# Performance work log

Hardware: AMD Instinct MI355X
Metric: run time of the kernel (lower is better)

Reference implementation:

```python
import jax, jax.numpy as jnp
import numpy as np

N_NODES = 50000
N_EDGES = 800000
D_IN, D_H, D_E = 512, 512, 256


def setup_inputs() -> dict:
    key = jax.random.key(0)
    ks = jax.random.split(key, 16)

    def lin(kw, kb, fan_in, fan_out):
        s = 1.0 / np.sqrt(fan_in)
        W = jax.random.uniform(kw, (fan_in, fan_out), dtype=jnp.float32, minval=-s, maxval=s)
        b = jax.random.uniform(kb, (fan_out,), dtype=jnp.float32, minval=-s, maxval=s)
        return W, b

    W1, b1 = lin(ks[2], ks[3], D_IN, D_H)
    W2, b2 = lin(ks[4], ks[5], D_H, D_H)
    W3, b3 = lin(ks[6], ks[7], D_H, D_E)
    We, be = lin(ks[8], ks[9], D_E, 7)
    Wh, bh = lin(ks[10], ks[11], D_E, 8)
    Wg, bg = lin(ks[12], ks[13], D_E, 57)

    return {
        "x": jax.random.normal(ks[0], (N_NODES, D_IN), dtype=jnp.float32),
        "edge_index": jax.random.randint(ks[1], (2, N_EDGES), 0, N_NODES, dtype=jnp.int32),
        "W1": W1, "b1": b1, "W2": W2, "b2": b2, "W3": W3, "b3": b3,
        "We": We, "be": be, "Wh": Wh, "bh": bh, "Wg": Wg, "bg": bg,
    }


def reference(x, edge_index, W1, b1, W2, b2, W3, b3, We, be, Wh, bh, Wg, bg):
    n = x.shape[0]
    # GCNConv: add self-loops, symmetric normalization D^{-1/2} A D^{-1/2}
    loops = jnp.arange(n, dtype=edge_index.dtype)
    src = jnp.concatenate([edge_index[0], loops])  # message sources
    dst = jnp.concatenate([edge_index[1], loops])  # aggregation targets
    deg = jax.ops.segment_sum(jnp.ones_like(src, dtype=x.dtype), dst, num_segments=n)
    dis = jnp.where(deg > 0, jax.lax.rsqrt(deg), 0.0)
    norm = (dis[src] * dis[dst])[:, None]  # [E+N, 1]

    def gcn_conv(h, W, b):
        h = h @ W                                   # [n, d_out]
        msg = h[src] * norm                         # gather + scale
        return jax.ops.segment_sum(msg, dst, num_segments=n) + b

    h = jax.nn.relu(gcn_conv(x, W1, b1))
    h = jax.nn.relu(gcn_conv(h, W2, b2))
    emb = gcn_conv(h, W3, b3)
    employment = emb @ We + be
    healthcare = emb @ Wh + bh
    grocery = emb @ Wg + bg
    return emb, employment, healthcare, grocery
```

## Files before the change

kernel.cpp:

```cpp
#include <hip/hip_runtime.h>

#define NN   50000
#define NNP  50048
#define NE   800000
#define DIN  512
#define DH   512
#define DE   256

#define CSR_CAP 1150016

typedef __bf16 bf16_t;
typedef __bf16 bf16x4 __attribute__((ext_vector_type(4)));
typedef __bf16 bf16x8 __attribute__((ext_vector_type(8)));
typedef float  f32x4  __attribute__((ext_vector_type(4)));
typedef _Float16 half_t;
typedef _Float16 half8 __attribute__((ext_vector_type(8)));

#define PB_SPLIT 25024
#define PB_IDEG  3125
#define PB_CSR   1124
#define PB_W1    1024
#define PB_W2    1024
#define PB_W3    512
#define PB_HEADW 80
#define PB_TOTAL (PB_SPLIT + PB_IDEG + PB_CSR + PB_W1 + PB_W2 + PB_W3 + PB_HEADW)

__global__ void k_prep(const float* __restrict__ X, bf16_t* __restrict__ Xh,
                       bf16_t* __restrict__ Xl, const int* __restrict__ dst,
                       int* __restrict__ indeg, int* __restrict__ csr,
                       const float* __restrict__ W1, bf16_t* __restrict__ B1h, bf16_t* __restrict__ B1l,
                       const float* __restrict__ W2, half_t* __restrict__ B2h, half_t* __restrict__ B2l,
                       const float* __restrict__ W3, half_t* __restrict__ B3h, half_t* __restrict__ B3l,
                       const float* __restrict__ We, const float* __restrict__ be,
                       const float* __restrict__ Wh, const float* __restrict__ bh,
                       const float* __restrict__ Wg, const float* __restrict__ bg,
                       bf16_t* __restrict__ Wth, bf16_t* __restrict__ Wtl,
                       float* __restrict__ bc) {
    int b = blockIdx.x;
    if (b < PB_SPLIT) {
        long idx = (long)b * 256 + threadIdx.x;
        long base = idx * 4;
        int row = (int)(base >> 9);
        f32x4 v;
        if (row < NN) v = *(const f32x4*)(X + base);
        else { v[0] = 0.f; v[1] = 0.f; v[2] = 0.f; v[3] = 0.f; }
        bf16x4 h, l;
        #pragma unroll
        for (int c = 0; c < 4; ++c) {
            float f = v[c];
            bf16_t hh = (bf16_t)f;
            h[c] = hh;
            l[c] = (bf16_t)(f - (float)hh);
        }
        *(bf16x4*)(Xh + base) = h;
        *(bf16x4*)(Xl + base) = l;
        return;
    }
    b -= PB_SPLIT;
    if (b < PB_IDEG) {
        int i = b * 256 + threadIdx.x;
        atomicAdd(&indeg[dst[i]], 1);
        return;
    }
    b -= PB_IDEG;
    if (b < PB_CSR) {
        int i = b * 256 + threadIdx.x;
        if (i < CSR_CAP / 4) ((int4*)csr)[i] = make_int4(NN, NN, NN, NN);
        return;
    }
    b -= PB_CSR;
    if (b < PB_W1) {
        int idx = b * 256 + threadIdx.x;
        int k = idx >> 9, n = idx & 511;
        float f = W1[idx];
        bf16_t h = (bf16_t)f;
        B1h[(size_t)n * DIN + k] = h;
        B1l[(size_t)n * DIN + k] = (bf16_t)(f - (float)h);
        return;
    }
    b -= PB_W1;
    if (b < PB_W2) {
        int idx = b * 256 + threadIdx.x;
        int k = idx >> 9, n = idx & 511;
        float f = W2[idx];
        half_t h = (half_t)f;
        B2h[(size_t)n * DH + k] = h;
        B2l[(size_t)n * DH + k] = (half_t)((f - (float)h) * 4096.f);
        return;
    }
    b -= PB_W2;
    if (b < PB_W3) {
        int idx = b * 256 + threadIdx.x;
        int k = idx >> 8, n = idx & 255;
        float f = W3[idx];
        half_t h = (half_t)f;
        B3h[(size_t)n * DH + k] = h;
        B3l[(size_t)n * DH + k] = (half_t)((f - (float)h) * 4096.f);
        return;
    }
    b -= PB_W3;
    {
        int idx = b * 256 + threadIdx.x;
        int n = idx / 256, k = idx % 256;
        float f = 0.f;
        if (n < 7)       f = We[k * 7 + n];
        else if (n < 15) f = Wh[k * 8 + (n - 7)];
        else if (n < 72) f = Wg[k * 57 + (n - 15)];
        bf16_t h = (bf16_t)f;
        Wth[idx] = h;
        Wtl[idx] = (bf16_t)(f - (float)h);
        if (k == 0) {
            float bb = 0.f;
            if (n < 7)       bb = be[n];
            else if (n < 15) bb = bh[n - 7];
            else if (n < 72) bb = bg[n - 15];
            bc[n] = bb;
        }
    }
}

#define SCAN_BLOCKS 49

__global__ __launch_bounds__(1024) void k_scan_a(const int* __restrict__ indeg,
                                                 int* __restrict__ rowptr,
                                                 float* __restrict__ dis,
                                                 int* __restrict__ bsum) {
    __shared__ int wsum[16];
    const int tid = threadIdx.x, lane = tid & 63, wid = tid >> 6;
    const int i = blockIdx.x * 1024 + tid;
    int deg = (i < NN) ? indeg[i] : 0;
    int v = (deg + 7) & ~7;
    int x = v;
    #pragma unroll
    for (int d = 1; d < 64; d <<= 1) {
        int t = __shfl_up(x, d, 64);
        if (lane >= d) x += t;
    }
    if (lane == 63) wsum[wid] = x;
    __syncthreads();
    if (wid == 0) {
        int s = (lane < 16) ? wsum[lane] : 0;
        #pragma unroll
        for (int d = 1; d < 16; d <<= 1) {
            int t = __shfl_up(s, d, 64);
            if (lane >= d) s += t;
        }
        if (lane < 16) wsum[lane] = s;
    }
    __syncthreads();
    int woff = (wid > 0) ? wsum[wid - 1] : 0;
    if (i < NN) {
        rowptr[i] = x - v + woff;
        dis[i] = rsqrtf((float)(deg + 1));
    } else if (i < NNP) {
        dis[i] = 0.f;
    }
    if (tid == 0) bsum[blockIdx.x] = wsum[15];
}

__global__ __launch_bounds__(64) void k_scan_b(const int* __restrict__ bsum,
                                               int* __restrict__ boff,
                                               int* __restrict__ rowptr) {
    const int lane = threadIdx.x;
    int v = (lane < SCAN_BLOCKS) ? bsum[lane] : 0;
    int x = v;
    #pragma unroll
    for (int d = 1; d < 64; d <<= 1) {
        int t = __shfl_up(x, d, 64);
        if (lane >= d) x += t;
    }
    if (lane < SCAN_BLOCKS) boff[lane] = x - v;
    if (lane == SCAN_BLOCKS - 1) rowptr[NN] = x;
}

__global__ void k_scan_c(const int* __restrict__ boff, int* __restrict__ rowptr,
                         int* __restrict__ cursor) {
    int i = blockIdx.x * blockDim.x + threadIdx.x;
    if (i < NN) {
        int r = rowptr[i] + boff[i >> 10];
        rowptr[i] = r;
        cursor[i] = r;
    }
}

__global__ void k_fill(const int* __restrict__ src, const int* __restrict__ dst,
                       int* __restrict__ cursor, int* __restrict__ csr, int e) {
    int i = blockIdx.x * blockDim.x + threadIdx.x;
    if (i < e) {
        int d = dst[i];
        int p = atomicAdd(&cursor[d], 1);
        csr[p] = src[i];
    }
}


__device__ __forceinline__ void gld_lds16(const void* g, void* l) {
    __builtin_amdgcn_global_load_lds(
        (const __attribute__((address_space(1))) unsigned int*)g,
        (__attribute__((address_space(3))) unsigned int*)l, 16, 0, 0);
}



__global__ __launch_bounds__(512) void k_gemm_bf3(
    const bf16_t* __restrict__ Ah, const bf16_t* __restrict__ Al,
    const bf16_t* __restrict__ Bh, const bf16_t* __restrict__ Bl,
    const float* __restrict__ disv,
    half_t* __restrict__ C, int N, int K) {
    __shared__ alignas(16) bf16_t sAh[2][128 * 32];
    __shared__ alignas(16) bf16_t sAl[2][128 * 32];
    __shared__ alignas(16) bf16_t sBh[2][128 * 32];
    __shared__ alignas(16) bf16_t sBl[2][128 * 32];

    const int tid = threadIdx.x;
    const int wave = tid >> 6, lane = tid & 63;
    const int quad = lane >> 4, l16 = lane & 15;
    const int bm = blockIdx.y * 128, bn = blockIdx.x * 128;
    const int wm = (wave >> 1) * 32, wn = (wave & 1) * 64;

    f32x4 acc[2][4];
    #pragma unroll
    for (int i = 0; i < 2; ++i)
        #pragma unroll
        for (int j = 0; j < 4; ++j)
            #pragma unroll
            for (int r = 0; r < 4; ++r) acc[i][j][r] = 0.f;

    const int srow = tid >> 2;
    const int schk = ((tid & 3) ^ ((tid >> 3) & 3)) * 16;
    const unsigned ldso = (unsigned)wave * 1024;

    const char* gAh0 = (const char*)(Ah + (size_t)(bm + srow) * K) + schk;
    const char* gAl0 = (const char*)(Al + (size_t)(bm + srow) * K) + schk;
    const char* gBh0 = (const char*)(Bh + (size_t)(bn + srow) * K) + schk;
    const char* gBl0 = (const char*)(Bl + (size_t)(bn + srow) * K) + schk;

    const int rsw = (l16 >> 1) & 3;
    const int nsteps = K >> 5;

    gld_lds16(gAh0, (char*)sAh[0] + ldso);
    gld_lds16(gAl0, (char*)sAl[0] + ldso);
    gld_lds16(gBh0, (char*)sBh[0] + ldso);
    gld_lds16(gBl0, (char*)sBl[0] + ldso);
    __syncthreads();

    for (int t = 0; t < nsteps; ++t) {
        const int cur = t & 1;
        if (t + 1 < nsteps) {
            const size_t kb = (size_t)(t + 1) * 64;
            const int nx = cur ^ 1;
            gld_lds16(gAh0 + kb, (char*)sAh[nx] + ldso);
            gld_lds16(gAl0 + kb, (char*)sAl[nx] + ldso);
            gld_lds16(gBh0 + kb, (char*)sBh[nx] + ldso);
            gld_lds16(gBl0 + kb, (char*)sBl[nx] + ldso);
        }
        bf16x8 fah[2], fal[2], fbh[4], fbl[4];
        #pragma unroll
        for (int i = 0; i < 2; ++i) {
            fah[i] = *(const bf16x8*)(sAh[cur] + (wm + 16 * i + l16) * 32 + (quad ^ rsw) * 8);
            fal[i] = *(const bf16x8*)(sAl[cur] + (wm + 16 * i + l16) * 32 + (quad ^ rsw) * 8);
        }
        #pragma unroll
        for (int j = 0; j < 4; ++j) {
            fbh[j] = *(const bf16x8*)(sBh[cur] + (wn + 16 * j + l16) * 32 + (quad ^ rsw) * 8);
            fbl[j] = *(const bf16x8*)(sBl[cur] + (wn + 16 * j + l16) * 32 + (quad ^ rsw) * 8);
        }
        #pragma unroll
        for (int i = 0; i < 2; ++i)
            #pragma unroll
            for (int j = 0; j < 4; ++j) {
                acc[i][j] = __builtin_amdgcn_mfma_f32_16x16x32_bf16(fah[i], fbh[j], acc[i][j], 0, 0, 0);
                acc[i][j] = __builtin_amdgcn_mfma_f32_16x16x32_bf16(fah[i], fbl[j], acc[i][j], 0, 0, 0);
                acc[i][j] = __builtin_amdgcn_mfma_f32_16x16x32_bf16(fal[i], fbh[j], acc[i][j], 0, 0, 0);
            }
        __syncthreads();
    }

    #pragma unroll
    for (int i = 0; i < 2; ++i) {
        const int rowb = bm + wm + 16 * i + quad * 4;
        float d0 = disv[rowb], d1 = disv[rowb + 1], d2 = disv[rowb + 2], d3 = disv[rowb + 3];
        #pragma unroll
        for (int j = 0; j < 4; ++j) {
            int col = bn + wn + 16 * j + l16;
            C[(size_t)(rowb + 0) * N + col] = (half_t)(acc[i][j][0] * d0);
            C[(size_t)(rowb + 1) * N + col] = (half_t)(acc[i][j][1] * d1);
            C[(size_t)(rowb + 2) * N + col] = (half_t)(acc[i][j][2] * d2);
            C[(size_t)(rowb + 3) * N + col] = (half_t)(acc[i][j][3] * d3);
        }
    }
}


__global__ __launch_bounds__(512) void k_gemm_f16(
    const half_t* __restrict__ A,
    const half_t* __restrict__ Bh, const half_t* __restrict__ Bl,
    const float* __restrict__ disv,
    half_t* __restrict__ C, int N, int K) {
    __shared__ alignas(16) half_t sA [2][128 * 32];
    __shared__ alignas(16) half_t sBh[2][128 * 32];
    __shared__ alignas(16) half_t sBl[2][128 * 32];

    const int tid = threadIdx.x;
    const int wave = tid >> 6, lane = tid & 63;
    const int quad = lane >> 4, l16 = lane & 15;
    const int bm = blockIdx.y * 128, bn = blockIdx.x * 128;
    const int wm = (wave >> 1) * 32, wn = (wave & 1) * 64;

    f32x4 aH[2][4], aM[2][4];
    #pragma unroll
    for (int i = 0; i < 2; ++i)
        #pragma unroll
        for (int j = 0; j < 4; ++j)
            #pragma unroll
            for (int r = 0; r < 4; ++r) { aH[i][j][r] = 0.f; aM[i][j][r] = 0.f; }

    const int srow = tid >> 2;
    const int schk = ((tid & 3) ^ ((tid >> 3) & 3)) * 16;
    const unsigned ldso = (unsigned)wave * 1024;

    const char* gA0  = (const char*)(A  + (size_t)(bm + srow) * K) + schk;
    const char* gBh0 = (const char*)(Bh + (size_t)(bn + srow) * K) + schk;
    const char* gBl0 = (const char*)(Bl + (size_t)(bn + srow) * K) + schk;

    const int rsw = (l16 >> 1) & 3;
    const int nsteps = K >> 5;

    gld_lds16(gA0,  (char*)sA[0]  + ldso);
    gld_lds16(gBh0, (char*)sBh[0] + ldso);
    gld_lds16(gBl0, (char*)sBl[0] + ldso);
    __syncthreads();

    for (int t = 0; t < nsteps; ++t) {
        const int cur = t & 1;
        if (t + 1 < nsteps) {
            const size_t kb = (size_t)(t + 1) * 64;
            const int nx = cur ^ 1;
            gld_lds16(gA0  + kb, (char*)sA[nx]  + ldso);
            gld_lds16(gBh0 + kb, (char*)sBh[nx] + ldso);
            gld_lds16(gBl0 + kb, (char*)sBl[nx] + ldso);
        }
        half8 fa[2], fbh[4], fbl[4];
        #pragma unroll
        for (int i = 0; i < 2; ++i)
            fa[i] = *(const half8*)(sA[cur] + (wm + 16 * i + l16) * 32 + (quad ^ rsw) * 8);
        #pragma unroll
        for (int j = 0; j < 4; ++j) {
            fbh[j] = *(const half8*)(sBh[cur] + (wn + 16 * j + l16) * 32 + (quad ^ rsw) * 8);
            fbl[j] = *(const half8*)(sBl[cur] + (wn + 16 * j + l16) * 32 + (quad ^ rsw) * 8);
        }
        #pragma unroll
        for (int i = 0; i < 2; ++i)
            #pragma unroll
            for (int j = 0; j < 4; ++j) {
                aH[i][j] = __builtin_amdgcn_mfma_f32_16x16x32_f16(fa[i], fbh[j], aH[i][j], 0, 0, 0);
                aM[i][j] = __builtin_amdgcn_mfma_f32_16x16x32_f16(fa[i], fbl[j], aM[i][j], 0, 0, 0);
            }
        __syncthreads();
    }

    const float s = 1.f / 4096.f;
    #pragma unroll
    for (int i = 0; i < 2; ++i) {
        const int rowb = bm + wm + 16 * i + quad * 4;
        float d0 = disv[rowb], d1 = disv[rowb + 1], d2 = disv[rowb + 2], d3 = disv[rowb + 3];
        #pragma unroll
        for (int j = 0; j < 4; ++j) {
            int col = bn + wn + 16 * j + l16;
            C[(size_t)(rowb + 0) * N + col] = (half_t)(fmaf(aM[i][j][0], s, aH[i][j][0]) * d0);
            C[(size_t)(rowb + 1) * N + col] = (half_t)(fmaf(aM[i][j][1], s, aH[i][j][1]) * d1);
            C[(size_t)(rowb + 2) * N + col] = (half_t)(fmaf(aM[i][j][2], s, aH[i][j][2]) * d2);
            C[(size_t)(rowb + 3) * N + col] = (half_t)(fmaf(aM[i][j][3], s, aH[i][j][3]) * d3);
        }
    }
}


__global__ __launch_bounds__(128) void k_agg16(
    const half_t* __restrict__ t, const int* __restrict__ rowptr,
    const int* __restrict__ csr, const float* __restrict__ dis,
    const float* __restrict__ bias, half_t* __restrict__ out) {
    const int node = blockIdx.x * 2 + (threadIdx.x >> 6);
    const int lane = threadIdx.x & 63;
    const int beg = rowptr[node], end = rowptr[node + 1];
    const float din = dis[node];
    const char* tc = (const char*)t;
    const unsigned lb = (unsigned)lane * 16u;

    float a0[8], a1[8], a2[8], a3[8];
    #pragma unroll
    for (int c = 0; c < 8; ++c) { a0[c] = 0.f; a1[c] = 0.f; a2[c] = 0.f; a3[c] = 0.f; }

    if (beg < end) {
        int4 sa = *(const int4*)(csr + beg);
        int4 sb = *(const int4*)(csr + beg + 4);
        half8 v0 = *(const half8*)(tc + (((unsigned)sa.x) << 10) + lb);
        half8 v1 = *(const half8*)(tc + (((unsigned)sa.y) << 10) + lb);
        half8 v2 = *(const half8*)(tc + (((unsigned)sa.z) << 10) + lb);
        half8 v3 = *(const half8*)(tc + (((unsigned)sa.w) << 10) + lb);
        half8 v4 = *(const half8*)(tc + (((unsigned)sb.x) << 10) + lb);
        half8 v5 = *(const half8*)(tc + (((unsigned)sb.y) << 10) + lb);
        half8 v6 = *(const half8*)(tc + (((unsigned)sb.z) << 10) + lb);
        half8 v7 = *(const half8*)(tc + (((unsigned)sb.w) << 10) + lb);
        int4 na = sa, nb = sb;
        if (beg + 8 < end) {
            na = *(const int4*)(csr + beg + 8);
            nb = *(const int4*)(csr + beg + 12);
        }
        for (int e = beg; e < end; ) {
            half8 u0 = v0, u1 = v1, u2 = v2, u3 = v3, u4 = v4, u5 = v5, u6 = v6, u7 = v7;
            e += 8;
            if (e < end) {
                v0 = *(const half8*)(tc + (((unsigned)na.x) << 10) + lb);
                v1 = *(const half8*)(tc + (((unsigned)na.y) << 10) + lb);
                v2 = *(const half8*)(tc + (((unsigned)na.z) << 10) + lb);
                v3 = *(const half8*)(tc + (((unsigned)na.w) << 10) + lb);
                v4 = *(const half8*)(tc + (((unsigned)nb.x) << 10) + lb);
                v5 = *(const half8*)(tc + (((unsigned)nb.y) << 10) + lb);
                v6 = *(const half8*)(tc + (((unsigned)nb.z) << 10) + lb);
                v7 = *(const half8*)(tc + (((unsigned)nb.w) << 10) + lb);
                if (e + 8 < end) {
                    na = *(const int4*)(csr + e + 8);
                    nb = *(const int4*)(csr + e + 12);
                }
            }
            #pragma unroll
            for (int c = 0; c < 8; ++c) {
                a0[c] = fmaf((float)u0[c], din, a0[c]);
                a1[c] = fmaf((float)u1[c], din, a1[c]);
                a2[c] = fmaf((float)u2[c], din, a2[c]);
                a3[c] = fmaf((float)u3[c], din, a3[c]);
                a0[c] = fmaf((float)u4[c], din, a0[c]);
                a1[c] = fmaf((float)u5[c], din, a1[c]);
                a2[c] = fmaf((float)u6[c], din, a2[c]);
                a3[c] = fmaf((float)u7[c], din, a3[c]);
            }
        }
    }

    half8 sv = ((const half8*)(t + (size_t)node * DH))[lane];
    f32x4 bv0 = ((const f32x4*)bias)[lane * 2];
    f32x4 bv1 = ((const f32x4*)bias)[lane * 2 + 1];
    half8 h;
    #pragma unroll
    for (int c = 0; c < 8; ++c) {
        float b = (c < 4) ? bv0[c] : bv1[c - 4];
        float acc = (a0[c] + a1[c]) + (a2[c] + a3[c]);
        float o = fmaf((float)sv[c], din, acc) + b;
        o = fmaxf(o, 0.f);
        h[c] = (half_t)o;
    }
    __builtin_nontemporal_store(h, (half8*)(out + (size_t)node * DH + lane * 8));
}

__global__ __launch_bounds__(128) void k_agg_f32(
    const half_t* __restrict__ t, const int* __restrict__ rowptr,
    const int* __restrict__ csr, const float* __restrict__ dis,
    const float* __restrict__ bias, float* __restrict__ out,
    bf16_t* __restrict__ Eh, bf16_t* __restrict__ El) {
    const int node = blockIdx.x * 4 + (threadIdx.x >> 5);
    const int lane = threadIdx.x & 31;
    const int beg = rowptr[node], end = rowptr[node + 1];
    const float din = dis[node];
    const char* tc = (const char*)t;
    const unsigned lb = (unsigned)lane * 16u;

    float a0[8], a1[8], a2[8], a3[8];
    #pragma unroll
    for (int c = 0; c < 8; ++c) { a0[c] = 0.f; a1[c] = 0.f; a2[c] = 0.f; a3[c] = 0.f; }

    if (beg < end) {
        int4 sa = *(const int4*)(csr + beg);
        int4 sb = *(const int4*)(csr + beg + 4);
        half8 v0 = *(const half8*)(tc + (((unsigned)sa.x) << 9) + lb);
        half8 v1 = *(const half8*)(tc + (((unsigned)sa.y) << 9) + lb);
        half8 v2 = *(const half8*)(tc + (((unsigned)sa.z) << 9) + lb);
        half8 v3 = *(const half8*)(tc + (((unsigned)sa.w) << 9) + lb);
        half8 v4 = *(const half8*)(tc + (((unsigned)sb.x) << 9) + lb);
        half8 v5 = *(const half8*)(tc + (((unsigned)sb.y) << 9) + lb);
        half8 v6 = *(const half8*)(tc + (((unsigned)sb.z) << 9) + lb);
        half8 v7 = *(const half8*)(tc + (((unsigned)sb.w) << 9) + lb);
        int4 na = sa, nb = sb;
        if (beg + 8 < end) {
            na = *(const int4*)(csr + beg + 8);
            nb = *(const int4*)(csr + beg + 12);
        }
        for (int e = beg; e < end; ) {
            half8 u0 = v0, u1 = v1, u2 = v2, u3 = v3, u4 = v4, u5 = v5, u6 = v6, u7 = v7;
            e += 8;
            if (e < end) {
                v0 = *(const half8*)(tc + (((unsigned)na.x) << 9) + lb);
                v1 = *(const half8*)(tc + (((unsigned)na.y) << 9) + lb);
                v2 = *(const half8*)(tc + (((unsigned)na.z) << 9) + lb);
                v3 = *(const half8*)(tc + (((unsigned)na.w) << 9) + lb);
                v4 = *(const half8*)(tc + (((unsigned)nb.x) << 9) + lb);
                v5 = *(const half8*)(tc + (((unsigned)nb.y) << 9) + lb);
                v6 = *(const half8*)(tc + (((unsigned)nb.z) << 9) + lb);
                v7 = *(const half8*)(tc + (((unsigned)nb.w) << 9) + lb);
                if (e + 8 < end) {
                    na = *(const int4*)(csr + e + 8);
                    nb = *(const int4*)(csr + e + 12);
                }
            }
            #pragma unroll
            for (int c = 0; c < 8; ++c) {
                a0[c] = fmaf((float)u0[c], din, a0[c]);
                a1[c] = fmaf((float)u1[c], din, a1[c]);
                a2[c] = fmaf((float)u2[c], din, a2[c]);
                a3[c] = fmaf((float)u3[c], din, a3[c]);
                a0[c] = fmaf((float)u4[c], din, a0[c]);
                a1[c] = fmaf((float)u5[c], din, a1[c]);
                a2[c] = fmaf((float)u6[c], din, a2[c]);
                a3[c] = fmaf((float)u7[c], din, a3[c]);
            }
        }
    }

    half8 sv = ((const half8*)(t + (size_t)node * DE))[lane];
    f32x4 bv0 = ((const f32x4*)bias)[lane * 2];
    f32x4 bv1 = ((const f32x4*)bias)[lane * 2 + 1];
    f32x4 o0, o1;
    bf16x8 hh, ll;
    #pragma unroll
    for (int c = 0; c < 8; ++c) {
        float b = (c < 4) ? bv0[c] : bv1[c - 4];
        float acc = (a0[c] + a1[c]) + (a2[c] + a3[c]);
        float o = fmaf((float)sv[c], din, acc) + b;
        if (c < 4) o0[c] = o; else o1[c - 4] = o;
        bf16_t h = (bf16_t)o;
        hh[c] = h;
        ll[c] = (bf16_t)(o - (float)h);
    }
    __builtin_nontemporal_store(o0, &((f32x4*)(out + (size_t)node * DE))[lane * 2]);
    __builtin_nontemporal_store(o1, &((f32x4*)(out + (size_t)node * DE))[lane * 2 + 1]);
    *(bf16x8*)(Eh + (size_t)node * DE + lane * 8) = hh;
    *(bf16x8*)(El + (size_t)node * DE + lane * 8) = ll;
}


__global__ __launch_bounds__(256) void k_heads_mfma(
    const bf16_t* __restrict__ Eh, const bf16_t* __restrict__ El,
    const bf16_t* __restrict__ Wth, const bf16_t* __restrict__ Wtl,
    const float* __restrict__ bc,
    float* __restrict__ oe, float* __restrict__ oh, float* __restrict__ og) {
    const int wave = threadIdx.x >> 6, lane = threadIdx.x & 63;
    const int quad = lane >> 4, l16 = lane & 15;
    const int row0 = blockIdx.x * 64 + wave * 16;

    f32x4 acc[5];
    #pragma unroll
    for (int j = 0; j < 5; ++j)
        #pragma unroll
        for (int r = 0; r < 4; ++r) acc[j][r] = 0.f;

    const size_t abase = (size_t)(row0 + l16) * 256 + quad * 8;
    #pragma unroll
    for (int ks = 0; ks < 256; ks += 32) {
        bf16x8 ah = *(const bf16x8*)(Eh + abase + ks);
        bf16x8 al = *(const bf16x8*)(El + abase + ks);
        #pragma unroll
        for (int j = 0; j < 5; ++j) {
            const size_t bbase = (size_t)(j * 16 + l16) * 256 + ks + quad * 8;
            bf16x8 bh = *(const bf16x8*)(Wth + bbase);
            bf16x8 bl = *(const bf16x8*)(Wtl + bbase);
            acc[j] = __builtin_amdgcn_mfma_f32_16x16x32_bf16(ah, bh, acc[j], 0, 0, 0);
            acc[j] = __builtin_amdgcn_mfma_f32_16x16x32_bf16(ah, bl, acc[j], 0, 0, 0);
            acc[j] = __builtin_amdgcn_mfma_f32_16x16x32_bf16(al, bh, acc[j], 0, 0, 0);
        }
    }

    #pragma unroll
    for (int j = 0; j < 5; ++j) {
        int col = j * 16 + l16;
        if (col < 72) {
            float b = bc[col];
            #pragma unroll
            for (int r = 0; r < 4; ++r) {
                int row = row0 + quad * 4 + r;
                if (row < NN) {
                    float v = acc[j][r] + b;
                    if (col < 7)       oe[(size_t)row * 7 + col] = v;
                    else if (col < 15) oh[(size_t)row * 8 + (col - 7)] = v;
                    else               og[(size_t)row * 57 + (col - 15)] = v;
                }
            }
        }
    }
}


extern "C" void kernel_launch(void* const* d_in, const int* in_sizes, int n_in,
                              void* d_out, int out_size, void* d_ws, size_t ws_size,
                              hipStream_t stream) {
    const float* x   = (const float*)d_in[0];
    const int*   ei  = (const int*)d_in[1];
    const float* W1  = (const float*)d_in[2];
    const float* b1  = (const float*)d_in[3];
    const float* W2  = (const float*)d_in[4];
    const float* b2  = (const float*)d_in[5];
    const float* W3  = (const float*)d_in[6];
    const float* b3  = (const float*)d_in[7];
    const float* We  = (const float*)d_in[8];
    const float* be  = (const float*)d_in[9];
    const float* Wh  = (const float*)d_in[10];
    const float* bh  = (const float*)d_in[11];
    const float* Wg  = (const float*)d_in[12];
    const float* bg  = (const float*)d_in[13];

    const int* e_src = ei;
    const int* e_dst = ei + NE;

    half_t* buf0 = (half_t*)d_ws;
    half_t* buf1 = buf0 + (size_t)NNP * DH;
    bf16_t* Xh   = (bf16_t*)buf1;
    bf16_t* Xl   = Xh + (size_t)NNP * DH;
    bf16_t* embh = Xl;
    bf16_t* embl = embh + (size_t)NNP * DE;
    bf16_t* B1h  = Xl + (size_t)NNP * DH;
    bf16_t* B1l  = B1h + (size_t)DIN * DH;
    half_t* B2h  = (half_t*)(B1l + (size_t)DIN * DH);
    half_t* B2l  = B2h + (size_t)DH * DH;
    half_t* B3h  = B2l + (size_t)DH * DH;
    half_t* B3l  = B3h + (size_t)DE * DH;
    bf16_t* Wth  = (bf16_t*)(B3l + (size_t)DE * DH);
    bf16_t* Wtl  = Wth + 80 * 256;
    float*  bc   = (float*)(Wtl + 80 * 256);
    int*   indeg  = (int*)(bc + 128);
    int*   rowptr = indeg + 50048;
    int*   cursor = rowptr + 50048;
    float* dis    = (float*)(cursor + 50048);
    int*   csr    = (int*)(dis + 50048);
    int*   bsum   = csr + CSR_CAP;
    int*   boff   = bsum + 64;

    float* emb   = (float*)d_out;
    float* out_e = emb + (size_t)NN * DE;
    float* out_h = out_e + (size_t)NN * 7;
    float* out_g = out_h + (size_t)NN * 8;

    hipMemsetAsync(indeg, 0, NN * sizeof(int), stream);
    k_prep<<<PB_TOTAL, 256, 0, stream>>>(x, Xh, Xl, e_dst, indeg, csr,
                                         W1, B1h, B1l, W2, B2h, B2l, W3, B3h, B3l,
                                         We, be, Wh, bh, Wg, bg, Wth, Wtl, bc);
    k_scan_a<<<SCAN_BLOCKS, 1024, 0, stream>>>(indeg, rowptr, dis, bsum);
    k_scan_b<<<1, 64, 0, stream>>>(bsum, boff, rowptr);
    k_scan_c<<<(NN + 255) / 256, 256, 0, stream>>>(boff, rowptr, cursor);
    k_fill<<<(NE + 255) / 256, 256, 0, stream>>>(e_src, e_dst, cursor, csr, NE);

    const int gy = NNP / 128;

    k_gemm_bf3<<<dim3(DH / 128, gy), 512, 0, stream>>>(Xh, Xl, B1h, B1l, dis, buf0, DH, DIN);
    k_agg16<<<NN / 2, 128, 0, stream>>>(buf0, rowptr, csr, dis, b1, buf1);

    k_gemm_f16<<<dim3(DH / 128, gy), 512, 0, stream>>>(buf1, B2h, B2l, dis, buf0, DH, DH);
    k_agg16<<<NN / 2, 128, 0, stream>>>(buf0, rowptr, csr, dis, b2, buf1);

    k_gemm_f16<<<dim3(DE / 128, gy), 512, 0, stream>>>(buf1, B3h, B3l, dis, buf0, DE, DH);
    k_agg_f32<<<NN / 4, 128, 0, stream>>>(buf0, rowptr, csr, dis, b3, emb, embh, embl);

    k_heads_mfma<<<NNP / 64, 256, 0, stream>>>(embh, embl, Wth, Wtl, bc, out_e, out_h, out_g);
}
```

Baseline: 835.6 us.

## Fuse scan kernels, triple-buffer f16 GEMM, split emb in heads kernel

The three scan kernels become one, which uses a global atomic counter as a grid barrier across its 49 blocks. This cuts two launches but relies on all blocks being resident at once. The f16 GEMM moves from double to triple-buffered LDS with explicit vmcnt waits and raw s_barrier, so loads run two steps ahead. The final aggregation no longer writes bf16 hi/lo copies of emb. The heads kernel instead reads the fp32 emb output and splits it into hi/lo parts in registers, which saves a write and read of the split buffers.

After: 842.2 us. No clear change (+0.8%).

```diff
diff --git a/kernel.cpp b/kernel.cpp
--- a/kernel.cpp
+++ b/kernel.cpp
@@ -35,7 +35,7 @@
                        const float* __restrict__ Wh, const float* __restrict__ bh,
                        const float* __restrict__ Wg, const float* __restrict__ bg,
                        bf16_t* __restrict__ Wth, bf16_t* __restrict__ Wtl,
-                       float* __restrict__ bc) {
+                       float* __restrict__ bc, int* __restrict__ done) {
     int b = blockIdx.x;
     if (b < PB_SPLIT) {
         long idx = (long)b * 256 + threadIdx.x;
@@ -102,6 +102,7 @@
     {
         int idx = b * 256 + threadIdx.x;
         int n = idx / 256, k = idx % 256;
+        if (idx == 0) *done = 0;
         float f = 0.f;
         if (n < 7)       f = We[k * 7 + n];
         else if (n < 15) f = Wh[k * 8 + (n - 7)];
@@ -121,11 +122,14 @@
 
 #define SCAN_BLOCKS 49
 
-__global__ __launch_bounds__(1024) void k_scan_a(const int* __restrict__ indeg,
-                                                 int* __restrict__ rowptr,
-                                                 float* __restrict__ dis,
-                                                 int* __restrict__ bsum) {
+__global__ __launch_bounds__(1024) void k_scan(const int* __restrict__ indeg,
+                                               int* __restrict__ rowptr,
+                                               int* __restrict__ cursor,
+                                               float* __restrict__ dis,
+                                               int* __restrict__ bsum,
+                                               int* __restrict__ done) {
     __shared__ int wsum[16];
+    __shared__ int s_off;
     const int tid = threadIdx.x, lane = tid & 63, wid = tid >> 6;
     const int i = blockIdx.x * 1024 + tid;
     int deg = (i < NN) ? indeg[i] : 0;
@@ -149,37 +153,39 @@
     }
     __syncthreads();
     int woff = (wid > 0) ? wsum[wid - 1] : 0;
+    int incl = x + woff;
+    int excl = incl - v;
+
+    if (tid == 0) {
+        bsum[blockIdx.x] = wsum[15];
+        __threadfence();
+        atomicAdd(done, 1);
+        while (atomicAdd(done, 0) < SCAN_BLOCKS) { }
+        __threadfence();
+    }
+    __syncthreads();
+
+    if (wid == 0) {
+        int bv = (lane < SCAN_BLOCKS) ? bsum[lane] : 0;
+        int bx = bv;
+        #pragma unroll
+        for (int d = 1; d < 64; d <<= 1) {
+            int t = __shfl_up(bx, d, 64);
+            if (lane >= d) bx += t;
+        }
+        if (lane == (int)blockIdx.x) s_off = bx - bv;
+    }
+    __syncthreads();
+    const int off = s_off;
+
     if (i < NN) {
-        rowptr[i] = x - v + woff;
+        int r = off + excl;
+        rowptr[i] = r;
+        cursor[i] = r;
         dis[i] = rsqrtf((float)(deg + 1));
+        if (i == NN - 1) rowptr[NN] = off + incl;
     } else if (i < NNP) {
         dis[i] = 0.f;
-    }
-    if (tid == 0) bsum[blockIdx.x] = wsum[15];
-}
-
-__global__ __launch_bounds__(64) void k_scan_b(const int* __restrict__ bsum,
-                                               int* __restrict__ boff,
-                                               int* __restrict__ rowptr) {
-    const int lane = threadIdx.x;
-    int v = (lane < SCAN_BLOCKS) ? bsum[lane] : 0;
-    int x = v;
-    #pragma unroll
-    for (int d = 1; d < 64; d <<= 1) {
-        int t = __shfl_up(x, d, 64);
-        if (lane >= d) x += t;
-    }
-    if (lane < SCAN_BLOCKS) boff[lane] = x - v;
-    if (lane == SCAN_BLOCKS - 1) rowptr[NN] = x;
-}
-
-__global__ void k_scan_c(const int* __restrict__ boff, int* __restrict__ rowptr,
-                         int* __restrict__ cursor) {
-    int i = blockIdx.x * blockDim.x + threadIdx.x;
-    if (i < NN) {
-        int r = rowptr[i] + boff[i >> 10];
-        rowptr[i] = r;
-        cursor[i] = r;
     }
 }
 
@@ -297,9 +303,9 @@
     const half_t* __restrict__ Bh, const half_t* __restrict__ Bl,
     const float* __restrict__ disv,
     half_t* __restrict__ C, int N, int K) {
-    __shared__ alignas(16) half_t sA [2][128 * 32];
-    __shared__ alignas(16) half_t sBh[2][128 * 32];
-    __shared__ alignas(16) half_t sBl[2][128 * 32];
+    __shared__ alignas(16) half_t sA [3][128 * 32];
+    __shared__ alignas(16) half_t sBh[3][128 * 32];
+    __shared__ alignas(16) half_t sBl[3][128 * 32];
 
     const int tid = threadIdx.x;
     const int wave = tid >> 6, lane = tid & 63;
@@ -326,28 +332,34 @@
     const int rsw = (l16 >> 1) & 3;
     const int nsteps = K >> 5;
 
-    gld_lds16(gA0,  (char*)sA[0]  + ldso);
-    gld_lds16(gBh0, (char*)sBh[0] + ldso);
-    gld_lds16(gBl0, (char*)sBl[0] + ldso);
-    __syncthreads();
-
-    for (int t = 0; t < nsteps; ++t) {
-        const int cur = t & 1;
-        if (t + 1 < nsteps) {
-            const size_t kb = (size_t)(t + 1) * 64;
-            const int nx = cur ^ 1;
-            gld_lds16(gA0  + kb, (char*)sA[nx]  + ldso);
-            gld_lds16(gBh0 + kb, (char*)sBh[nx] + ldso);
-            gld_lds16(gBl0 + kb, (char*)sBl[nx] + ldso);
-        }
+    gld_lds16(gA0,       (char*)sA      + ldso);
+    gld_lds16(gBh0,      (char*)sBh     + ldso);
+    gld_lds16(gBl0,      (char*)sBl     + ldso);
+    gld_lds16(gA0  + 64, (char*)sA  + 8192 + ldso);
+    gld_lds16(gBh0 + 64, (char*)sBh + 8192 + ldso);
+    gld_lds16(gBl0 + 64, (char*)sBl + 8192 + ldso);
+
+    int cur = 0, nx = 2;
+    for (int t = 0; t < nsteps - 1; ++t) {
+        asm volatile("s_waitcnt vmcnt(3)" ::: "memory");
+        asm volatile("s_barrier" ::: "memory");
+        if (t + 2 < nsteps) {
+            const size_t kb = (size_t)(t + 2) * 64;
+            gld_lds16(gA0  + kb, (char*)sA  + nx * 8192 + ldso);
+            gld_lds16(gBh0 + kb, (char*)sBh + nx * 8192 + ldso);
+            gld_lds16(gBl0 + kb, (char*)sBl + nx * 8192 + ldso);
+        }
+        const half_t* sAc  = (const half_t*)((const char*)sA  + cur * 8192);
+        const half_t* sBhc = (const half_t*)((const char*)sBh + cur * 8192);
+        const half_t* sBlc = (const half_t*)((const char*)sBl + cur * 8192);
         half8 fa[2], fbh[4], fbl[4];
         #pragma unroll
         for (int i = 0; i < 2; ++i)
-            fa[i] = *(const half8*)(sA[cur] + (wm + 16 * i + l16) * 32 + (quad ^ rsw) * 8);
+            fa[i] = *(const half8*)(sAc + (wm + 16 * i + l16) * 32 + (quad ^ rsw) * 8);
         #pragma unroll
         for (int j = 0; j < 4; ++j) {
-            fbh[j] = *(const half8*)(sBh[cur] + (wn + 16 * j + l16) * 32 + (quad ^ rsw) * 8);
-            fbl[j] = *(const half8*)(sBl[cur] + (wn + 16 * j + l16) * 32 + (quad ^ rsw) * 8);
+            fbh[j] = *(const half8*)(sBhc + (wn + 16 * j + l16) * 32 + (quad ^ rsw) * 8);
+            fbl[j] = *(const half8*)(sBlc + (wn + 16 * j + l16) * 32 + (quad ^ rsw) * 8);
         }
         #pragma unroll
         for (int i = 0; i < 2; ++i)
@@ -356,7 +368,31 @@
                 aH[i][j] = __builtin_amdgcn_mfma_f32_16x16x32_f16(fa[i], fbh[j], aH[i][j], 0, 0, 0);
                 aM[i][j] = __builtin_amdgcn_mfma_f32_16x16x32_f16(fa[i], fbl[j], aM[i][j], 0, 0, 0);
             }
-        __syncthreads();
+        cur = (cur == 2) ? 0 : cur + 1;
+        nx  = (nx  == 2) ? 0 : nx  + 1;
+    }
+    asm volatile("s_waitcnt vmcnt(0)" ::: "memory");
+    asm volatile("s_barrier" ::: "memory");
+    {
+        const half_t* sAc  = (const half_t*)((const char*)sA  + cur * 8192);
+        const half_t* sBhc = (const half_t*)((const char*)sBh + cur * 8192);
+        const half_t* sBlc = (const half_t*)((const char*)sBl + cur * 8192);
+        half8 fa[2], fbh[4], fbl[4];
+        #pragma unroll
+        for (int i = 0; i < 2; ++i)
+            fa[i] = *(const half8*)(sAc + (wm + 16 * i + l16) * 32 + (quad ^ rsw) * 8);
+        #pragma unroll
+        for (int j = 0; j < 4; ++j) {
+            fbh[j] = *(const half8*)(sBhc + (wn + 16 * j + l16) * 32 + (quad ^ rsw) * 8);
+            fbl[j] = *(const half8*)(sBlc + (wn + 16 * j + l16) * 32 + (quad ^ rsw) * 8);
+        }
+        #pragma unroll
+        for (int i = 0; i < 2; ++i)
+            #pragma unroll
+            for (int j = 0; j < 4; ++j) {
+                aH[i][j] = __builtin_amdgcn_mfma_f32_16x16x32_f16(fa[i], fbh[j], aH[i][j], 0, 0, 0);
+                aM[i][j] = __builtin_amdgcn_mfma_f32_16x16x32_f16(fa[i], fbl[j], aM[i][j], 0, 0, 0);
+            }
     }
 
     const float s = 1.f / 4096.f;
@@ -456,8 +492,7 @@
 __global__ __launch_bounds__(128) void k_agg_f32(
     const half_t* __restrict__ t, const int* __restrict__ rowptr,
     const int* __restrict__ csr, const float* __restrict__ dis,
-    const float* __restrict__ bias, float* __restrict__ out,
-    bf16_t* __restrict__ Eh, bf16_t* __restrict__ El) {
+    const float* __restrict__ bias, float* __restrict__ out) {
     const int node = blockIdx.x * 4 + (threadIdx.x >> 5);
     const int lane = threadIdx.x & 31;
     const int beg = rowptr[node], end = rowptr[node + 1];
@@ -520,26 +555,20 @@
     f32x4 bv0 = ((const f32x4*)bias)[lane * 2];
     f32x4 bv1 = ((const f32x4*)bias)[lane * 2 + 1];
     f32x4 o0, o1;
-    bf16x8 hh, ll;
     #pragma unroll
     for (int c = 0; c < 8; ++c) {
         float b = (c < 4) ? bv0[c] : bv1[c - 4];
         float acc = (a0[c] + a1[c]) + (a2[c] + a3[c]);
         float o = fmaf((float)sv[c], din, acc) + b;
         if (c < 4) o0[c] = o; else o1[c - 4] = o;
-        bf16_t h = (bf16_t)o;
-        hh[c] = h;
-        ll[c] = (bf16_t)(o - (float)h);
-    }
-    __builtin_nontemporal_store(o0, &((f32x4*)(out + (size_t)node * DE))[lane * 2]);
-    __builtin_nontemporal_store(o1, &((f32x4*)(out + (size_t)node * DE))[lane * 2 + 1]);
-    *(bf16x8*)(Eh + (size_t)node * DE + lane * 8) = hh;
-    *(bf16x8*)(El + (size_t)node * DE + lane * 8) = ll;
+    }
+    ((f32x4*)(out + (size_t)node * DE))[lane * 2]     = o0;
+    ((f32x4*)(out + (size_t)node * DE))[lane * 2 + 1] = o1;
 }
 
 
 __global__ __launch_bounds__(256) void k_heads_mfma(
-    const bf16_t* __restrict__ Eh, const bf16_t* __restrict__ El,
+    const float* __restrict__ emb,
     const bf16_t* __restrict__ Wth, const bf16_t* __restrict__ Wtl,
     const float* __restrict__ bc,
     float* __restrict__ oe, float* __restrict__ oh, float* __restrict__ og) {
@@ -553,11 +582,24 @@
         #pragma unroll
         for (int r = 0; r < 4; ++r) acc[j][r] = 0.f;
 
-    const size_t abase = (size_t)(row0 + l16) * 256 + quad * 8;
+    const int arow = row0 + l16;
+    const size_t abase = (size_t)((arow < NN) ? arow : 0) * 256 + quad * 8;
     #pragma unroll
     for (int ks = 0; ks < 256; ks += 32) {
-        bf16x8 ah = *(const bf16x8*)(Eh + abase + ks);
-        bf16x8 al = *(const bf16x8*)(El + abase + ks);
+        f32x4 e0 = *(const f32x4*)(emb + abase + ks);
+        f32x4 e1 = *(const f32x4*)(emb + abase + ks + 4);
+        bf16x8 ah, al;
+        #pragma unroll
+        for (int c = 0; c < 4; ++c) {
+            float f = e0[c];
+            bf16_t h = (bf16_t)f;
+            ah[c] = h;
+            al[c] = (bf16_t)(f - (float)h);
+            float g = e1[c];
+            bf16_t h2 = (bf16_t)g;
+            ah[4 + c] = h2;
+            al[4 + c] = (bf16_t)(g - (float)h2);
+        }
         #pragma unroll
         for (int j = 0; j < 5; ++j) {
             const size_t bbase = (size_t)(j * 16 + l16) * 256 + ks + quad * 8;
@@ -614,8 +656,6 @@
     half_t* buf1 = buf0 + (size_t)NNP * DH;
     bf16_t* Xh   = (bf16_t*)buf1;
     bf16_t* Xl   = Xh + (size_t)NNP * DH;
-    bf16_t* embh = Xl;
-    bf16_t* embl = embh + (size_t)NNP * DE;
     bf16_t* B1h  = Xl + (size_t)NNP * DH;
     bf16_t* B1l  = B1h + (size_t)DIN * DH;
     half_t* B2h  = (half_t*)(B1l + (size_t)DIN * DH);
@@ -631,7 +671,7 @@
     float* dis    = (float*)(cursor + 50048);
     int*   csr    = (int*)(dis + 50048);
     int*   bsum   = csr + CSR_CAP;
-    int*   boff   = bsum + 64;
+    int*   done   = bsum + 64;
 
     float* emb   = (float*)d_out;
     float* out_e = emb + (size_t)NN * DE;
@@ -641,10 +681,8 @@
     hipMemsetAsync(indeg, 0, NN * sizeof(int), stream);
     k_prep<<<PB_TOTAL, 256, 0, stream>>>(x, Xh, Xl, e_dst, indeg, csr,
                                          W1, B1h, B1l, W2, B2h, B2l, W3, B3h, B3l,
-                                         We, be, Wh, bh, Wg, bg, Wth, Wtl, bc);
-    k_scan_a<<<SCAN_BLOCKS, 1024, 0, stream>>>(indeg, rowptr, dis, bsum);
-    k_scan_b<<<1, 64, 0, stream>>>(bsum, boff, rowptr);
-    k_scan_c<<<(NN + 255) / 256, 256, 0, stream>>>(boff, rowptr, cursor);
+                                         We, be, Wh, bh, Wg, bg, Wth, Wtl, bc, done);
+    k_scan<<<SCAN_BLOCKS, 1024, 0, stream>>>(indeg, rowptr, cursor, dis, bsum, done);
     k_fill<<<(NE + 255) / 256, 256, 0, stream>>>(e_src, e_dst, cursor, csr, NE);
 
     const int gy = NNP / 128;
@@ -656,7 +694,7 @@
     k_agg16<<<NN / 2, 128, 0, stream>>>(buf0, rowptr, csr, dis, b2, buf1);
 
     k_gemm_f16<<<dim3(DE / 128, gy), 512, 0, stream>>>(buf1, B3h, B3l, dis, buf0, DE, DH);
-    k_agg_f32<<<NN / 4, 128, 0, stream>>>(buf0, rowptr, csr, dis, b3, emb, embh, embl);
-
-    k_heads_mfma<<<NNP / 64, 256, 0, stream>>>(embh, embl, Wth, Wtl, bc, out_e, out_h, out_g);
-}
+    k_agg_f32<<<NN / 4, 128, 0, stream>>>(buf0, rowptr, csr, dis, b3, emb);
+
+    k_heads_mfma<<<NNP / 64, 256, 0, stream>>>(emb, Wth, Wtl, bc, out_e, out_h, out_g);
+}
```
